# Performance work log

Measured on AMD Instinct MI355X. Metric: run time of the kernel, lower is better.

The kernel has to match this reference:

```python
import jax, jax.numpy as jnp
import numpy as np

B, S, DIM, H = 2, 2048, 1024, 16
DH = DIM // H


def setup_inputs() -> dict:
    key = jax.random.key(0)
    ks = jax.random.split(key, 12)
    sd = 0.02
    inp = {
        "query": jax.random.normal(ks[0], (B, S, DIM), jnp.float32),
        "key": jax.random.normal(ks[1], (B, S, DIM), jnp.float32),
        "value": jax.random.normal(ks[2], (B, S, DIM), jnp.float32),
        "pad_mask": jax.random.randint(ks[3], (B, 1, 1, S), 0, 2, jnp.int32),
        "training_status": 1,
        "Wq": jax.random.normal(ks[4], (DIM, DIM), jnp.float32) * sd,
        "bq": jnp.zeros((DIM,), jnp.float32),
        "Wk": jax.random.normal(ks[5], (DIM, DIM), jnp.float32) * sd,
        "bk": jnp.zeros((DIM,), jnp.float32),
        "Wv": jax.random.normal(ks[6], (DIM, DIM), jnp.float32) * sd,
        "bv": jnp.zeros((DIM,), jnp.float32),
        "Wf": jax.random.normal(ks[7], (DIM, DIM), jnp.float32) * sd,
        "bf": jnp.zeros((DIM,), jnp.float32),
    }
    return inp


def reference(query, key, value, pad_mask, training_status, Wq, bq, Wk, bk, Wv, bv, Wf, bf):
    b, s, _ = query.shape
    # projections, split heads -> [B, H, S, Dh]
    def split_heads(x):
        return x.reshape(b, -1, H, DH).transpose(0, 2, 1, 3)

    q = split_heads(query @ Wq + bq)
    k = split_heads(key @ Wk + bk)
    v = split_heads(value @ Wv + bv)

    # NOTE: original divides by sqrt(Dh) twice (explicit + self.scale) => /Dh
    scores = jnp.einsum("bhqd,bhkd->bhqk", q, k) / jnp.asarray(DH, q.dtype)
    if training_status:
        scores = jnp.where(pad_mask == 0, jnp.asarray(-1e9, scores.dtype), scores)
    attn = jax.nn.softmax(scores, axis=-1)
    out = jnp.einsum("bhqk,bhkd->bhqd", attn, v)  # [B,H,S,Dh]
    out = out.transpose(0, 2, 1, 3).reshape(b, s, DIM)
    return out @ Wf + bf
```

## Files before the change

### kernel.cpp

```cpp
#include <hip/hip_runtime.h>

#define Bn   2
#define Sn   2048
#define DIMn 1024
#define Hn   16
#define DHn  64

typedef unsigned short u16;
typedef unsigned int   u32;

typedef __attribute__((ext_vector_type(8))) __bf16 bf16x8;
typedef __attribute__((ext_vector_type(8))) float  f32x8v;
typedef __attribute__((ext_vector_type(4))) float  f32x4;

__device__ __forceinline__ u16 f2bf(float f) {
    union { float f; u32 u; } v; v.f = f;
    u32 r = v.u + 0x7fffu + ((v.u >> 16) & 1u);
    return (u16)(r >> 16);
}
__device__ __forceinline__ bf16x8 ldfrag(const u16* p) {
    union { uint4 u; bf16x8 v; } x;
    x.u = *(const uint4*)p;
    return x.v;
}
__device__ __forceinline__ uint4 pack8(const u16 h[8]) {
    uint4 r;
    r.x = (u32)h[0] | ((u32)h[1] << 16);
    r.y = (u32)h[2] | ((u32)h[3] << 16);
    r.z = (u32)h[4] | ((u32)h[5] << 16);
    r.w = (u32)h[6] | ((u32)h[7] << 16);
    return r;
}
__device__ __forceinline__ void gl_lds16(const void* g, void* l) {
    __builtin_amdgcn_global_load_lds(
        (const __attribute__((address_space(1))) void*)g,
        (__attribute__((address_space(3))) void*)l, 16, 0, 0);
}
__device__ __forceinline__ void barrier_nodrain() {
    asm volatile("" ::: "memory");
    __builtin_amdgcn_s_barrier();
    asm volatile("" ::: "memory");
}

__global__ __launch_bounds__(256) void prep_weights(
    const float* __restrict__ Wq, const float* __restrict__ Wk,
    const float* __restrict__ Wv, const float* __restrict__ Wf,
    u16* __restrict__ Wt)
{
    __shared__ __align__(16) float tile[64][68];
    const float* W = (blockIdx.z == 0) ? Wq : (blockIdx.z == 1) ? Wk
                   : (blockIdx.z == 2) ? Wv : Wf;
    const int t = threadIdx.x;
    const int n0 = blockIdx.x * 64, k0 = blockIdx.y * 64;
    const int rr = t >> 4, cc = (t & 15) * 4;
#pragma unroll
    for (int i = 0; i < 4; i++)
        *(float4*)&tile[rr + 16 * i][cc] =
            *(const float4*)(W + (size_t)(k0 + rr + 16 * i) * DIMn + n0 + cc);
    __syncthreads();
#pragma unroll
    for (int e = 0; e < 2; e++) {
        const int ci = 2 * t + e;
        const int nn = ci >> 3, kc = ci & 7;
        const int n = n0 + nn, k = k0 + kc * 8;
        u16 h[8];
#pragma unroll
        for (int j = 0; j < 8; j++) h[j] = f2bf(tile[kc * 8 + j][nn]);
        const int X = n >> 7, o = (n >> 4) & 7, l15 = n & 15;
        const int T = k >> 5, quad = (k >> 3) & 3;
        const size_t off =
            ((((size_t)(blockIdx.z * 8 + X) * 32 + T) * 8 + o) * 64 + quad * 16 + l15) * 8;
        *(uint4*)(Wt + off) = pack8(h);
    }
}

__global__ __launch_bounds__(256) void gemm_qkv(
    const float* __restrict__ Aq, const float* __restrict__ Ak,
    const float* __restrict__ Av, const u16* __restrict__ Wt,
    const float* __restrict__ bqp, const float* __restrict__ bkp,
    const float* __restrict__ bvp, u16* __restrict__ Qw,
    u16* __restrict__ Kw, u16* __restrict__ VwT)
{
    __shared__ union {
        struct { __align__(16) float Afp[2][4096];
                 __align__(16) u16   Bbf[2][4096]; } s;
        __align__(16) u16 Ep[32][144];
    } L;

    const int f = blockIdx.x;
    const int xcd = f & 7;
    const int q = f >> 3;
    const int z = q >> 5;
    const int rem = q & 31;
    const int yi = rem >> 3, x = rem & 7;
    const int y = xcd * 4 + yi;
    const int m0 = y * 128, n0 = x * 128;

    const float* A    = (z == 0) ? Aq  : (z == 1) ? Ak  : Av;
    const float* bias = (z == 0) ? bqp : (z == 1) ? bkp : bvp;

    const int t = threadIdx.x;
    const int lane = t & 63, wave = t >> 6;
    const int quad = lane >> 4, l15 = lane & 15;
    const int wm = wave >> 1, wn = wave & 1;

    const int r8 = lane >> 3, c8 = lane & 7;
    const float* baseA[4];
#pragma unroll
    for (int s = 0; s < 4; s++)
        baseA[s] = A + (size_t)(m0 + (wave * 4 + s) * 8 + r8) * DIMn + ((c8 ^ r8) << 2);
    const u16* baseB[2];
#pragma unroll
    for (int s = 0; s < 2; s++)
        baseB[s] = Wt + ((size_t)((z * 8 + x) * 32) * 8 + (wave * 2 + s)) * 512 + lane * 8;

    auto STAGE = [&](int tt, int buf) {
#pragma unroll
        for (int s = 0; s < 4; s++)
            gl_lds16(baseA[s] + tt * 32, &L.s.Afp[buf][(wave * 4 + s) * 256]);
#pragma unroll
        for (int s = 0; s < 2; s++)
            gl_lds16(baseB[s] + (size_t)tt * 4096, &L.s.Bbf[buf][(wave * 8 + s * 4) * 128]);
    };

    f32x4 acc[4][4];
#pragma unroll
    for (int i = 0; i < 4; i++)
#pragma unroll
        for (int j = 0; j < 4; j++) acc[i][j] = (f32x4){0.f, 0.f, 0.f, 0.f};

    const int NT = DIMn / 32;
    STAGE(0, 0);
    STAGE(1, 1);

#pragma unroll 2
    for (int tt = 0; tt < NT; ++tt) {
        const int buf = tt & 1;
        if (tt < NT - 1) asm volatile("s_waitcnt vmcnt(6)" ::: "memory");
        else             asm volatile("s_waitcnt vmcnt(0)" ::: "memory");
        barrier_nodrain();

        bf16x8 a[4], b[4];
#pragma unroll
        for (int i = 0; i < 4; i++) {
            const int lr = wm * 64 + i * 16 + l15;
            const int rx = lr & 7;
            union { struct { f32x4 lo, hi; } p; f32x8v v; } u;
            u.p.lo = *(const f32x4*)&L.s.Afp[buf][lr * 32 + (((quad * 2 + 0) ^ rx) << 2)];
            u.p.hi = *(const f32x4*)&L.s.Afp[buf][lr * 32 + (((quad * 2 + 1) ^ rx) << 2)];
            a[i] = __builtin_convertvector(u.v, bf16x8);
        }
#pragma unroll
        for (int j = 0; j < 4; j++)
            b[j] = ldfrag(&L.s.Bbf[buf][((wn * 4 + j) * 4 + quad) * 128 + l15 * 8]);
#pragma unroll
        for (int i = 0; i < 4; i++)
#pragma unroll
            for (int j = 0; j < 4; j++)
                acc[i][j] = __builtin_amdgcn_mfma_f32_16x16x32_bf16(a[i], b[j], acc[i][j], 0, 0, 0);

        asm volatile("s_waitcnt lgkmcnt(0)" ::: "memory");
        barrier_nodrain();
        if (tt + 2 < NT) STAGE(tt + 2, buf);
    }

    float bv[4];
#pragma unroll
    for (int j = 0; j < 4; j++) bv[j] = bias[n0 + wn * 64 + j * 16 + l15];

    const int bb = y >> 4;

    if (z == 0) {
#pragma unroll
        for (int i = 0; i < 4; i++) {
            __syncthreads();
#pragma unroll
            for (int j = 0; j < 4; j++)
#pragma unroll
                for (int r = 0; r < 4; r++)
                    L.Ep[wm * 16 + quad * 4 + r][wn * 64 + j * 16 + l15] =
                        f2bf(acc[i][j][r] + bv[j]);
            __syncthreads();
#pragma unroll
            for (int e = 0; e < 2; e++) {
                const int ci = t + 256 * e;
                const int row = ci >> 4, c = ci & 15;
                const uint4 v = *(const uint4*)&L.Ep[row][c * 8];
                const int m = m0 + (row >> 4) * 64 + i * 16 + (row & 15);
                const int ss = m & 2047;
                const int n = n0 + c * 8;
                const int hh = n >> 6, dd = n & 63;
                *(uint4*)(Qw + ((size_t)(bb * Hn + hh) * Sn + ss) * DHn + dd) = v;
            }
        }
    } else if (z == 1) {
#pragma unroll
        for (int i = 0; i < 4; i++) {
            __syncthreads();
#pragma unroll
            for (int j = 0; j < 4; j++)
#pragma unroll
                for (int r = 0; r < 4; r++)
                    L.Ep[wm * 16 + quad * 4 + r][wn * 64 + j * 16 + l15] =
                        f2bf(acc[i][j][r] + bv[j]);
            __syncthreads();
#pragma unroll
            for (int e2 = 0; e2 < 2; e2++) {
                const int tid = t + 256 * e2;
                const int l15o = tid & 15;
                const int qo   = (tid >> 4) & 3;
                const int k1   = (tid >> 6) & 1;
                const int c3   = (tid >> 7) & 1;
                const int w    = (tid >> 8) & 1;
                const int c    = c3 * 8 + k1 * 4 + qo;
                const uint4 v = *(const uint4*)&L.Ep[w * 16 + l15o][c * 8];
                const int ss = (m0 & 2047) + w * 64 + i * 16 + l15o;
                const int hh = (n0 + c * 8) >> 6;
                const int jt = ss >> 6;
                const int o  = i * 2 + k1;
                const size_t off =
                    ((((size_t)(bb * Hn + hh) * 32 + jt) * 8 + o) * 64 + qo * 16 + l15o) * 8;
                *(uint4*)(Kw + off) = v;
            }
        }
    } else {
#pragma unroll
        for (int j = 0; j < 4; j++) {
            __syncthreads();
#pragma unroll
            for (int i = 0; i < 4; i++) {
                u16 h4[4];
#pragma unroll
                for (int r = 0; r < 4; r++) h4[r] = f2bf(acc[i][j][r] + bv[j]);
                uint2 pk;
                pk.x = (u32)h4[0] | ((u32)h4[1] << 16);
                pk.y = (u32)h4[2] | ((u32)h4[3] << 16);
                *(uint2*)&L.Ep[wn * 16 + l15][wm * 64 + i * 16 + quad * 4] = pk;
            }
            __syncthreads();
#pragma unroll
            for (int e2 = 0; e2 < 2; e2++) {
                const int tid = t + 256 * e2;
                const int l15o = tid & 15;
                const int qo   = (tid >> 4) & 3;
                const int k1   = (tid >> 6) & 1;
                const int c3   = (tid >> 7) & 1;
                const int w    = (tid >> 8) & 1;
                const int c    = c3 * 8 + k1 * 4 + qo;
                const uint4 v = *(const uint4*)&L.Ep[w * 16 + l15o][c * 8];
                const int n  = n0 + w * 64 + j * 16 + l15o;
                const int hh = n >> 6;
                const int jt = ((m0 & 2047) >> 6) + c3;
                const int o  = j * 2 + k1;
                const size_t off =
                    ((((size_t)(bb * Hn + hh) * 32 + jt) * 8 + o) * 64 + qo * 16 + l15o) * 8;
                *(uint4*)(VwT + off) = v;
            }
        }
    }
}

__global__ __launch_bounds__(256) void gemm_final(
    const u16* __restrict__ A, const u16* __restrict__ Bt,
    const float* __restrict__ bias, float* __restrict__ out)
{
    __shared__ __align__(16) u16 Abf[3][32 * 128];
    __shared__ __align__(16) u16 Bbf[3][32 * 128];

    const int f = blockIdx.x;
    const int xcd = f & 7, q = f >> 3;
    const int y = xcd * 4 + (q >> 3), x = q & 7;
    const int m0 = y * 128, n0 = x * 128;

    const int t = threadIdx.x;
    const int lane = t & 63, wave = t >> 6;
    const int quad = lane >> 4, l15 = lane & 15;
    const int wm = wave >> 1, wn = wave & 1;

    int arow[2], aq[2];
#pragma unroll
    for (int s = 0; s < 2; s++) {
        const int c = wave * 8 + s * 4 + quad;
        arow[s] = (c >> 2) * 16 + l15;
        aq[s] = c & 3;
    }
    const u16* baseB[2];
#pragma unroll
    for (int s = 0; s < 2; s++)
        baseB[s] = Bt + ((size_t)(x * 32) * 8 + (wave * 2 + s)) * 512 + lane * 8;

    auto STAGE = [&](int tt, int buf) {
        const int hh = tt >> 1, d64 = (tt & 1) * 32;
#pragma unroll
        for (int s = 0; s < 2; s++) {
            const int m = m0 + arow[s], bb = m >> 11, ss = m & 2047;
            const u16* gp = A + ((size_t)(bb * Hn + hh) * Sn + ss) * DHn + d64 + aq[s] * 8;
            gl_lds16(gp, &Abf[buf][(wave * 8 + s * 4) * 128]);
        }
#pragma unroll
        for (int s = 0; s < 2; s++)
            gl_lds16(baseB[s] + (size_t)tt * 4096, &Bbf[buf][(wave * 8 + s * 4) * 128]);
    };

    f32x4 acc[4][4];
#pragma unroll
    for (int i = 0; i < 4; i++)
#pragma unroll
        for (int j = 0; j < 4; j++) acc[i][j] = (f32x4){0.f, 0.f, 0.f, 0.f};

    const int NT = DIMn / 32;
    STAGE(0, 0);
    STAGE(1, 1);
    STAGE(2, 2);

    int buf = 0;
    for (int tt = 0; tt < NT; ++tt) {
        if (tt < NT - 2)       asm volatile("s_waitcnt vmcnt(8)" ::: "memory");
        else if (tt == NT - 2) asm volatile("s_waitcnt vmcnt(4)" ::: "memory");
        else                   asm volatile("s_waitcnt vmcnt(0)" ::: "memory");
        barrier_nodrain();

        bf16x8 a[4], b[4];
#pragma unroll
        for (int i = 0; i < 4; i++)
            a[i] = ldfrag(&Abf[buf][((wm * 4 + i) * 4 + quad) * 128 + l15 * 8]);
#pragma unroll
        for (int j = 0; j < 4; j++)
            b[j] = ldfrag(&Bbf[buf][((wn * 4 + j) * 4 + quad) * 128 + l15 * 8]);
#pragma unroll
        for (int i = 0; i < 4; i++)
#pragma unroll
            for (int j = 0; j < 4; j++)
                acc[i][j] = __builtin_amdgcn_mfma_f32_16x16x32_bf16(a[i], b[j], acc[i][j], 0, 0, 0);

        asm volatile("s_waitcnt lgkmcnt(0)" ::: "memory");
        barrier_nodrain();
        if (tt + 3 < NT) STAGE(tt + 3, buf);
        buf = (buf == 2) ? 0 : buf + 1;
    }

    float bv[4];
#pragma unroll
    for (int j = 0; j < 4; j++) bv[j] = bias[n0 + wn * 64 + j * 16 + l15];

#pragma unroll
    for (int i = 0; i < 4; i++)
#pragma unroll
        for (int j = 0; j < 4; j++) {
            const int n = n0 + wn * 64 + j * 16 + l15;
#pragma unroll
            for (int r = 0; r < 4; r++) {
                const int m = m0 + wm * 64 + i * 16 + quad * 4 + r;
                out[(size_t)m * DIMn + n] = acc[i][j][r] + bv[j];
            }
        }
}

__global__ __launch_bounds__(256) void attn_mfma(
    const u16* __restrict__ Qw, const u16* __restrict__ Kw,
    const u16* __restrict__ VwT, const int* __restrict__ mask,
    const int* __restrict__ tstat, u16* __restrict__ Aw)
{
    __shared__ __align__(16) u16 Kbf[2][32 * 128];
    __shared__ __align__(16) u16 Vbf[2][32 * 128];
    __shared__ __align__(16) u16 Ps[64 * 64];

    const int f = blockIdx.x;
    const int xcd = f & 7, q = f >> 3;
    const int p = xcd * 4 + (q >> 5);
    const int qt = q & 31;
    const int b = p >> 4, h = p & 15;
    const int q0 = qt * 64;

    const int t = threadIdx.x;
    const int lane = t & 63, wave = t >> 6;
    const int quad = lane >> 4, l15 = lane & 15;
    const bool use_mask = (tstat[0] != 0);
    const size_t slab = (size_t)(b * Hn + h) * Sn * DHn;

    const size_t hbase = (size_t)(b * Hn + h) * 32 * 8 * 512;
    const u16* baseK[2];
    const u16* baseV[2];
#pragma unroll
    for (int s = 0; s < 2; s++) {
        const int o = wave * 2 + s;
        baseK[s] = Kw  + hbase + (size_t)o * 512 + lane * 8;
        baseV[s] = VwT + hbase + (size_t)o * 512 + lane * 8;
    }

    {
        const int4* msrc4 = (const int4*)(mask + (size_t)b * Sn);
        int4* mdst4 = (int4*)&Kbf[0][0];
        mdst4[t]       = msrc4[t];
        mdst4[t + 256] = msrc4[t + 256];
    }
    bf16x8 aq[2];
#pragma unroll
    for (int ks = 0; ks < 2; ks++) {
        union { uint4 u; bf16x8 v; } xx;
        xx.u = *(const uint4*)(Qw + slab + (size_t)(q0 + wave * 16 + l15) * DHn + ks * 32 + quad * 8);
        aq[ks] = xx.v;
    }
    __syncthreads();

    u32 mw0 = 0, mw1 = 0, mw2 = 0, mw3 = 0;
    {
        const int* ml = (const int*)&Kbf[0][0];
#pragma unroll
        for (int k = 0; k < 128; k++) {
            const u32 bit = (ml[k * 16 + l15] != 0) ? 1u : 0u;
            if (k < 32)      mw0 |= bit << k;
            else if (k < 64) mw1 |= bit << (k - 32);
            else if (k < 96) mw2 |= bit << (k - 64);
            else             mw3 |= bit << (k - 96);
        }
    }
    __syncthreads();

    auto STAGE = [&](int tt, int buf) {
#pragma unroll
        for (int s = 0; s < 2; s++) {
            gl_lds16(baseK[s] + (size_t)tt * 4096, &Kbf[buf][(wave * 8 + s * 4) * 128]);
            gl_lds16(baseV[s] + (size_t)tt * 4096, &Vbf[buf][(wave * 8 + s * 4) * 128]);
        }
    };

    float lsum[4] = {0.f, 0.f, 0.f, 0.f};
    f32x4 O[4];
#pragma unroll
    for (int dt = 0; dt < 4; dt++) O[dt] = (f32x4){0.f, 0.f, 0.f, 0.f};

    const int NT = Sn / 64;
    STAGE(0, 0);
    STAGE(1, 1);

#pragma unroll 2
    for (int tt = 0; tt < NT; ++tt) {
        const int buf = tt & 1;
        if (tt < NT - 1) asm volatile("s_waitcnt vmcnt(4)" ::: "memory");
        else             asm volatile("s_waitcnt vmcnt(0)" ::: "memory");
        barrier_nodrain();

        f32x4 s[4];
#pragma unroll
        for (int ct = 0; ct < 4; ct++) s[ct] = (f32x4){0.f, 0.f, 0.f, 0.f};
#pragma unroll
        for (int ct = 0; ct < 4; ct++)
#pragma unroll
            for (int ks = 0; ks < 2; ks++) {
                const bf16x8 bk = ldfrag(&Kbf[buf][(ct * 8 + ks * 4 + quad) * 128 + l15 * 8]);
                s[ct] = __builtin_amdgcn_mfma_f32_16x16x32_bf16(aq[ks], bk, s[ct], 0, 0, 0);
            }

        const int wsel = tt >> 3;
        const u32 cw = (wsel == 0) ? mw0 : (wsel == 1) ? mw1 : (wsel == 2) ? mw2 : mw3;
        const int sh = (tt & 7) * 4;
        u32 mc[4];
#pragma unroll
        for (int ct = 0; ct < 4; ct++)
            mc[ct] = use_mask ? ((cw >> (sh + ct)) & 1u) : 1u;

#pragma unroll
        for (int ct = 0; ct < 4; ct++)
#pragma unroll
            for (int r = 0; r < 4; r++) {
                const float sv = mc[ct] ? s[ct][r] * (1.0f / 64.0f) : -1e9f;
                const float pp = __expf(sv);
                lsum[r] += pp;
                const int prow = wave * 16 + quad * 4 + r;
                Ps[prow * 64 + ((ct * 16 + l15) ^ ((prow & 7) << 3))] = f2bf(pp);
            }
        asm volatile("s_waitcnt lgkmcnt(0)" ::: "memory");

        bf16x8 pa[2];
        const int rrow = wave * 16 + l15;
#pragma unroll
        for (int kc = 0; kc < 2; kc++)
            pa[kc] = ldfrag(&Ps[rrow * 64 + ((kc * 32 + quad * 8) ^ ((l15 & 7) << 3))]);
#pragma unroll
        for (int dt = 0; dt < 4; dt++)
#pragma unroll
            for (int kc = 0; kc < 2; kc++) {
                const bf16x8 bvv = ldfrag(&Vbf[buf][(dt * 8 + kc * 4 + quad) * 128 + l15 * 8]);
                O[dt] = __builtin_amdgcn_mfma_f32_16x16x32_bf16(pa[kc], bvv, O[dt], 0, 0, 0);
            }

        asm volatile("s_waitcnt lgkmcnt(0)" ::: "memory");
        barrier_nodrain();
        if (tt + 2 < NT) STAGE(tt + 2, buf);
    }

#pragma unroll
    for (int r = 0; r < 4; r++) {
#pragma unroll
        for (int off = 1; off < 16; off <<= 1) lsum[r] += __shfl_xor(lsum[r], off);
    }
    float linv[4];
#pragma unroll
    for (int r = 0; r < 4; r++) linv[r] = 1.0f / fmaxf(lsum[r], 1e-30f);

    __syncthreads();
#pragma unroll
    for (int r = 0; r < 4; r++)
#pragma unroll
        for (int dt = 0; dt < 4; dt++)
            Ps[(wave * 16 + quad * 4 + r) * 64 + dt * 16 + l15] = f2bf(O[dt][r] * linv[r]);
    __syncthreads();
#pragma unroll
    for (int e2 = 0; e2 < 2; e2++) {
        const int tid = t + 256 * e2;
        const int lr = tid >> 3, c16 = tid & 7;
        const uint4 v = *(const uint4*)&Ps[lr * 64 + c16 * 8];
        *(uint4*)(Aw + slab + (size_t)(q0 + lr) * DHn + c16 * 8) = v;
    }
}

extern "C" void kernel_launch(void* const* d_in, const int* in_sizes, int n_in,
                              void* d_out, int out_size, void* d_ws, size_t ws_size,
                              hipStream_t stream) {
    const float* query = (const float*)d_in[0];
    const float* key   = (const float*)d_in[1];
    const float* value = (const float*)d_in[2];
    const int*   pmask = (const int*)d_in[3];
    const int*   tstat = (const int*)d_in[4];
    const float* Wq  = (const float*)d_in[5];
    const float* bq  = (const float*)d_in[6];
    const float* Wk  = (const float*)d_in[7];
    const float* bk  = (const float*)d_in[8];
    const float* Wv  = (const float*)d_in[9];
    const float* bv  = (const float*)d_in[10];
    const float* Wf  = (const float*)d_in[11];
    const float* bfb = (const float*)d_in[12];
    float* outp = (float*)d_out;

    const size_t NT = (size_t)Bn * Sn * DIMn;
    u16* Qw  = (u16*)d_ws;
    u16* Kw  = Qw + NT;
    u16* VwT = Kw + NT;
    u16* Wt  = VwT + NT;
    const size_t WSZ = (size_t)DIMn * DIMn;

    prep_weights<<<dim3(16, 16, 4), 256, 0, stream>>>(Wq, Wk, Wv, Wf, Wt);

    gemm_qkv<<<768, 256, 0, stream>>>(query, key, value, Wt, bq, bk, bv, Qw, Kw, VwT);

    attn_mfma<<<1024, 256, 0, stream>>>(Qw, Kw, VwT, pmask, tstat, Qw);

    gemm_final<<<256, 256, 0, stream>>>(Qw, Wt + 3 * WSZ, bfb, outp);
}
```

Baseline: 277.8 us.

## Convert QKV A-tiles to bf16 in registers before LDS, add MFMA priority hints

The QKV GEMM used to load fp32 activations straight into LDS and convert them to bf16 on every fragment read. It now loads fp32 into registers, converts once and writes bf16 fragments into LDS in MFMA order. This halves A-tile LDS space and read traffic and drops the per-read swizzle and convert work. In exchange the register double-buffering adds VGPR pressure and puts the load latency on the wave's own waitcnt. The change also uses the hardware bf16 conversion in f2bf and wraps the attention MFMA blocks in s_setprio.

After: 278.0 us. No clear change (+0.1%).

```diff
diff --git a/kernel.cpp b/kernel.cpp
--- a/kernel.cpp
+++ b/kernel.cpp
@@ -14,9 +14,7 @@
 typedef __attribute__((ext_vector_type(4))) float  f32x4;
 
 __device__ __forceinline__ u16 f2bf(float f) {
-    union { float f; u32 u; } v; v.f = f;
-    u32 r = v.u + 0x7fffu + ((v.u >> 16) & 1u);
-    return (u16)(r >> 16);
+    union { __bf16 h; u16 u; } v; v.h = (__bf16)f; return v.u;
 }
 __device__ __forceinline__ bf16x8 ldfrag(const u16* p) {
     union { uint4 u; bf16x8 v; } x;
@@ -82,8 +80,8 @@
     u16* __restrict__ Kw, u16* __restrict__ VwT)
 {
     __shared__ union {
-        struct { __align__(16) float Afp[2][4096];
-                 __align__(16) u16   Bbf[2][4096]; } s;
+        struct { __align__(16) u16 Abf[2][4096];
+                 __align__(16) u16 Bbf[2][4096]; } s;
         __align__(16) u16 Ep[32][144];
     } L;
 
@@ -104,24 +102,38 @@
     const int quad = lane >> 4, l15 = lane & 15;
     const int wm = wave >> 1, wn = wave & 1;
 
-    const int r8 = lane >> 3, c8 = lane & 7;
-    const float* baseA[4];
-#pragma unroll
-    for (int s = 0; s < 4; s++)
-        baseA[s] = A + (size_t)(m0 + (wave * 4 + s) * 8 + r8) * DIMn + ((c8 ^ r8) << 2);
+    const float* baseA[2];
+#pragma unroll
+    for (int s = 0; s < 2; s++)
+        baseA[s] = A + (size_t)(m0 + (wave * 2 + s) * 16 + l15) * DIMn + quad * 8;
     const u16* baseB[2];
 #pragma unroll
     for (int s = 0; s < 2; s++)
         baseB[s] = Wt + ((size_t)((z * 8 + x) * 32) * 8 + (wave * 2 + s)) * 512 + lane * 8;
 
-    auto STAGE = [&](int tt, int buf) {
-#pragma unroll
-        for (int s = 0; s < 4; s++)
-            gl_lds16(baseA[s] + tt * 32, &L.s.Afp[buf][(wave * 4 + s) * 256]);
+    auto LOADA = [&](int tt, uint4 (&ar)[4]) {
+#pragma unroll
+        for (int s = 0; s < 2; s++) {
+            const float* p = baseA[s] + tt * 32;
+            ar[2 * s]     = *(const uint4*)(p);
+            ar[2 * s + 1] = *(const uint4*)(p + 4);
+        }
+    };
+    auto STAGEB = [&](int tt, int buf) {
 #pragma unroll
         for (int s = 0; s < 2; s++)
-            gl_lds16(baseB[s] + (size_t)tt * 4096, &L.s.Bbf[buf][(wave * 8 + s * 4) * 128]);
+            gl_lds16(baseB[s] + (size_t)tt * 4096, &L.s.Bbf[buf][(wave * 2 + s) * 512]);
     };
+    auto CVTWRITE = [&](uint4 (&ar)[4], int buf) {
+#pragma unroll
+        for (int s = 0; s < 2; s++) {
+            union { uint4 u[2]; f32x8v f; } cv;
+            cv.u[0] = ar[2 * s]; cv.u[1] = ar[2 * s + 1];
+            union { bf16x8 v; uint4 u; } hv;
+            hv.v = __builtin_convertvector(cv.f, bf16x8);
+            *(uint4*)&L.s.Abf[buf][(wave * 2 + s) * 512 + lane * 8] = hv.u;
+        }
+    };
 
     f32x4 acc[4][4];
 #pragma unroll
@@ -130,26 +142,21 @@
         for (int j = 0; j < 4; j++) acc[i][j] = (f32x4){0.f, 0.f, 0.f, 0.f};
 
     const int NT = DIMn / 32;
-    STAGE(0, 0);
-    STAGE(1, 1);
-
-#pragma unroll 2
-    for (int tt = 0; tt < NT; ++tt) {
-        const int buf = tt & 1;
+    uint4 ra[4], rb[4];
+    LOADA(0, ra); STAGEB(0, 0);
+    LOADA(1, rb); STAGEB(1, 1);
+
+    auto ITER = [&](int tt, uint4 (&ar)[4], int buf) {
         if (tt < NT - 1) asm volatile("s_waitcnt vmcnt(6)" ::: "memory");
         else             asm volatile("s_waitcnt vmcnt(0)" ::: "memory");
+        CVTWRITE(ar, buf);
+        asm volatile("s_waitcnt lgkmcnt(0)" ::: "memory");
         barrier_nodrain();
 
         bf16x8 a[4], b[4];
 #pragma unroll
-        for (int i = 0; i < 4; i++) {
-            const int lr = wm * 64 + i * 16 + l15;
-            const int rx = lr & 7;
-            union { struct { f32x4 lo, hi; } p; f32x8v v; } u;
-            u.p.lo = *(const f32x4*)&L.s.Afp[buf][lr * 32 + (((quad * 2 + 0) ^ rx) << 2)];
-            u.p.hi = *(const f32x4*)&L.s.Afp[buf][lr * 32 + (((quad * 2 + 1) ^ rx) << 2)];
-            a[i] = __builtin_convertvector(u.v, bf16x8);
-        }
+        for (int i = 0; i < 4; i++)
+            a[i] = ldfrag(&L.s.Abf[buf][((wm * 4 + i) * 4 + quad) * 128 + l15 * 8]);
 #pragma unroll
         for (int j = 0; j < 4; j++)
             b[j] = ldfrag(&L.s.Bbf[buf][((wn * 4 + j) * 4 + quad) * 128 + l15 * 8]);
@@ -161,8 +168,9 @@
 
         asm volatile("s_waitcnt lgkmcnt(0)" ::: "memory");
         barrier_nodrain();
-        if (tt + 2 < NT) STAGE(tt + 2, buf);
-    }
+        if (tt + 2 < NT) { LOADA(tt + 2, ar); STAGEB(tt + 2, buf); }
+    };
+    for (int tt = 0; tt < NT; tt += 2) { ITER(tt, ra, 0); ITER(tt + 1, rb, 1); }
 
     float bv[4];
 #pragma unroll
@@ -444,6 +452,7 @@
         f32x4 s[4];
 #pragma unroll
         for (int ct = 0; ct < 4; ct++) s[ct] = (f32x4){0.f, 0.f, 0.f, 0.f};
+        __builtin_amdgcn_s_setprio(1);
 #pragma unroll
         for (int ct = 0; ct < 4; ct++)
 #pragma unroll
@@ -451,6 +460,7 @@
                 const bf16x8 bk = ldfrag(&Kbf[buf][(ct * 8 + ks * 4 + quad) * 128 + l15 * 8]);
                 s[ct] = __builtin_amdgcn_mfma_f32_16x16x32_bf16(aq[ks], bk, s[ct], 0, 0, 0);
             }
+        __builtin_amdgcn_s_setprio(0);
 
         const int wsel = tt >> 3;
         const u32 cw = (wsel == 0) ? mw0 : (wsel == 1) ? mw1 : (wsel == 2) ? mw2 : mw3;
@@ -477,6 +487,7 @@
 #pragma unroll
         for (int kc = 0; kc < 2; kc++)
             pa[kc] = ldfrag(&Ps[rrow * 64 + ((kc * 32 + quad * 8) ^ ((l15 & 7) << 3))]);
+        __builtin_amdgcn_s_setprio(1);
 #pragma unroll
         for (int dt = 0; dt < 4; dt++)
 #pragma unroll
@@ -484,6 +495,7 @@
                 const bf16x8 bvv = ldfrag(&Vbf[buf][(dt * 8 + kc * 4 + quad) * 128 + l15 * 8]);
                 O[dt] = __builtin_amdgcn_mfma_f32_16x16x32_bf16(pa[kc], bvv, O[dt], 0, 0, 0);
             }
+        __builtin_amdgcn_s_setprio(0);
 
         asm volatile("s_waitcnt lgkmcnt(0)" ::: "memory");
         barrier_nodrain();
```
